# Kernel optimization log

Measured on AMD Instinct MI355X. Metric: run time of the kernel, lower is better.

The kernel has to match this reference:

```python
import jax, jax.numpy as jnp
import numpy as np

N_NODES = 100000
N_EDGES = 1600000
IN_F = 128
OUT_F = 64


def setup_inputs() -> dict:
    key = jax.random.key(0)
    ks = jax.random.split(key, 9)
    x = jax.random.normal(ks[0], (N_NODES, IN_F), dtype=jnp.float32)
    Wv = jax.random.normal(ks[1], (IN_F, OUT_F), dtype=jnp.float32) / np.sqrt(IN_F)
    bv = jax.random.normal(ks[2], (OUT_F,), dtype=jnp.float32) * 0.02
    wq = jax.random.normal(ks[3], (OUT_F,), dtype=jnp.float32) / np.sqrt(OUT_F)
    bq = jax.random.normal(ks[4], (1,), dtype=jnp.float32) * 0.02
    wk = jax.random.normal(ks[5], (OUT_F,), dtype=jnp.float32) / np.sqrt(OUT_F)
    bk = jax.random.normal(ks[6], (1,), dtype=jnp.float32) * 0.02
    src = jax.random.randint(ks[7], (N_EDGES,), 0, N_NODES, dtype=jnp.int64)
    dst = jax.random.randint(ks[8], (N_EDGES,), 0, N_NODES, dtype=jnp.int64)
    return {"x": x, "Wv": Wv, "bv": bv, "wq": wq, "bq": bq,
            "wk": wk, "bk": bk, "src": src, "dst": dst}


def reference(x, Wv, bv, wq, bq, wk, bk, src, dst):
    n = x.shape[0]
    # node transform (linear_v) and scalar scores (linear_q, linear_k)
    xv = x @ Wv + bv                      # [N, OUT_F]
    el = xv @ wq + bq[0]                  # [N] source score
    er = xv @ wk + bk[0]                  # [N] destination score
    # per-edge score: u_add_v + leaky_relu(0.2)
    e = jax.nn.leaky_relu(el[src] + er[dst], negative_slope=0.2)  # [E]
    # edge softmax over incoming edges of each dst (numerically stable)
    emax = jax.ops.segment_max(e, dst, num_segments=n)            # [N]
    ex = jnp.exp(e - emax[dst])                                   # [E]
    denom = jax.ops.segment_sum(ex, dst, num_segments=n)          # [N]
    attn = ex / denom[dst]                                        # [E]
    # u_mul_e + aggregate_sum: weighted scatter of source features into dst
    out = jax.ops.segment_sum(xv[src] * attn[:, None], dst, num_segments=n)
    return out
```

## Files before the change

kernel.cpp:

```cpp
#include <hip/hip_runtime.h>
#include <hip/hip_bf16.h>

#define NN 100000
#define NE 1600000
#define IN_F 128
#define OUT_F 64
#define NBINS 196
#define BIN_SHIFT 9
#define P1_WGS 391
#define NREP2 8
#define SUBCAP 1280

typedef __attribute__((ext_vector_type(8))) short bf16x8;
typedef __attribute__((ext_vector_type(4))) float f32x4;

__device__ __forceinline__ short f2bf(float f) {
  unsigned u = __float_as_uint(f);
  unsigned r = (u + 0x7fffu + ((u >> 16) & 1u)) >> 16;
  return (short)r;
}
__device__ __forceinline__ float bf2f(ushort u) {
  return __uint_as_float(((unsigned)u) << 16);
}

__global__ __launch_bounds__(256) void prep_w(
    const float* __restrict__ Wv, short* __restrict__ wvt) {
  const int i = blockIdx.x * 256 + threadIdx.x;
  if (i >= IN_F * OUT_F) return;
  const int j = i >> 7, k = i & 127;
  wvt[i] = f2bf(Wv[k * OUT_F + j]);
}

__global__ __launch_bounds__(256) void node_transform(
    const float* __restrict__ x, const short* __restrict__ wvt,
    const float* __restrict__ bv, const float* __restrict__ wq,
    const float* __restrict__ bq, const float* __restrict__ wk,
    const float* __restrict__ bk,
    ushort* __restrict__ xvb, float* __restrict__ el, float* __restrict__ er) {
  const int wave = threadIdx.x >> 6, lane = threadIdx.x & 63;
  const int node0 = blockIdx.x * 64 + wave * 16;
  const int j15 = lane & 15, g = lane >> 4;
  const int kb = g * 8;

  int row = node0 + j15;
  if (row >= NN) row = NN - 1;
  const float* xr = x + (size_t)row * IN_F;
  bf16x8 a[4];
#pragma unroll
  for (int kt = 0; kt < 4; ++kt) {
    const float4 f0 = *(const float4*)(xr + kt * 32 + kb);
    const float4 f1 = *(const float4*)(xr + kt * 32 + kb + 4);
    bf16x8 t;
    t[0] = f2bf(f0.x); t[1] = f2bf(f0.y); t[2] = f2bf(f0.z); t[3] = f2bf(f0.w);
    t[4] = f2bf(f1.x); t[5] = f2bf(f1.y); t[6] = f2bf(f1.z); t[7] = f2bf(f1.w);
    a[kt] = t;
  }

  bf16x8 b[16];
#pragma unroll
  for (int nt = 0; nt < 4; ++nt)
#pragma unroll
    for (int kt = 0; kt < 4; ++kt)
      b[nt * 4 + kt] = *(const bf16x8*)(wvt + (size_t)(nt * 16 + j15) * IN_F + kt * 32 + kb);

  f32x4 acc[4];
#pragma unroll
  for (int nt = 0; nt < 4; ++nt) acc[nt] = (f32x4){0.f, 0.f, 0.f, 0.f};
#pragma unroll
  for (int nt = 0; nt < 4; ++nt)
#pragma unroll
    for (int kt = 0; kt < 4; ++kt)
      acc[nt] = __builtin_amdgcn_mfma_f32_16x16x32_bf16(a[kt], b[nt * 4 + kt], acc[nt], 0, 0, 0);

  float bvl[4], wql[4], wkl[4];
#pragma unroll
  for (int nt = 0; nt < 4; ++nt) {
    bvl[nt] = bv[nt * 16 + j15];
    wql[nt] = wq[nt * 16 + j15];
    wkl[nt] = wk[nt * 16 + j15];
  }
  const float bq0 = bq[0], bk0 = bk[0];

#pragma unroll
  for (int r = 0; r < 4; ++r) {
    const int node = node0 + g * 4 + r;
    float pq = 0.f, pk = 0.f;
#pragma unroll
    for (int nt = 0; nt < 4; ++nt) {
      const float v = acc[nt][r] + bvl[nt];
      if (node < NN) xvb[(size_t)node * OUT_F + nt * 16 + j15] = (ushort)f2bf(v);
      pq += v * wql[nt];
      pk += v * wkl[nt];
    }
#pragma unroll
    for (int o = 1; o < 16; o <<= 1) {
      pq += __shfl_xor(pq, o);
      pk += __shfl_xor(pk, o);
    }
    if (j15 == 0 && node < NN) {
      el[node] = pq + bq0;
      er[node] = pk + bk0;
    }
  }
}

__global__ __launch_bounds__(256) void bin_pass1(
    const int* __restrict__ src, const int* __restrict__ dst,
    int* __restrict__ bincur, unsigned* __restrict__ slab) {
  __shared__ int hist[NBINS];
  __shared__ int base_[NBINS];
  const int t = threadIdx.x;
  const int rep = blockIdx.x & (NREP2 - 1);
  for (int i = t; i < NBINS; i += 256) hist[i] = 0;
  __syncthreads();
  const int e0 = blockIdx.x * 4096;
  int sv[16], dv[16];
#pragma unroll
  for (int r = 0; r < 16; ++r) {
    const int i = e0 + r * 256 + t;
    if (i < NE) {
      sv[r] = src[i];
      dv[r] = dst[i];
      atomicAdd(&hist[dv[r] >> BIN_SHIFT], 1);
    } else {
      sv[r] = -1;
      dv[r] = 0;
    }
  }
  __syncthreads();
  for (int b = t; b < NBINS; b += 256) {
    base_[b] = (hist[b] > 0) ? atomicAdd(&bincur[rep * NBINS + b], hist[b]) : 0;
    hist[b] = 0;
  }
  __syncthreads();
#pragma unroll
  for (int r = 0; r < 16; ++r) {
    if (sv[r] >= 0) {
      const int s = sv[r], d = dv[r];
      const int b = d >> BIN_SHIFT;
      const unsigned dl = (unsigned)(d & 511);
      const int pos = base_[b] + atomicAdd(&hist[b], 1);
      slab[(size_t)(b * NREP2 + rep) * SUBCAP + pos] = (dl << 17) | (unsigned)s;
    }
  }
}

__global__ __launch_bounds__(256) void bin_off_k(
    const int* __restrict__ bincur, int* __restrict__ binoff,
    int* __restrict__ off) {
  __shared__ int sp[256];
  const int t = threadIdx.x;
  int v = 0;
  if (t < NBINS) {
#pragma unroll
    for (int r = 0; r < NREP2; ++r) v += bincur[r * NBINS + t];
  }
  sp[t] = v;
  __syncthreads();
  for (int o = 1; o < 256; o <<= 1) {
    const int u = (t >= o) ? sp[t - o] : 0;
    __syncthreads();
    sp[t] += u;
    __syncthreads();
  }
  const int excl = sp[t] - v;
  if (t < NBINS) binoff[t] = excl;
  if (t == 0) { binoff[NBINS] = NE; off[NN] = NE; }
}

__global__ __launch_bounds__(256) void bin_scatter(
    const unsigned* __restrict__ slab, const int* __restrict__ bincur,
    const int* __restrict__ binoff, const float* __restrict__ el,
    const float* __restrict__ er, int* __restrict__ off,
    uint2* __restrict__ csr) {
  __shared__ int cnt2[512];
  __shared__ int sp[256];
  __shared__ float er_l[512];
  const int b = blockIdx.x, t = threadIdx.x;
  const int n0 = b << BIN_SHIFT;
  const int csr0 = binoff[b];

  cnt2[t] = 0; cnt2[t + 256] = 0;
  {
    const int n = n0 + t;
    er_l[t] = (n < NN) ? er[n] : 0.f;
    const int n2 = n0 + 256 + t;
    er_l[256 + t] = (n2 < NN) ? er[n2] : 0.f;
  }
  __syncthreads();

#pragma unroll
  for (int rep = 0; rep < NREP2; ++rep) {
    const int cnt = bincur[rep * NBINS + b];
    const unsigned* sl = slab + (size_t)(b * NREP2 + rep) * SUBCAP;
    for (int i = t; i < cnt; i += 256)
      atomicAdd(&cnt2[sl[i] >> 17], 1);
  }
  __syncthreads();

  const int c0 = cnt2[2 * t], c1 = cnt2[2 * t + 1];
  const int psum = c0 + c1;
  sp[t] = psum;
  __syncthreads();
  for (int o = 1; o < 256; o <<= 1) {
    const int u = (t >= o) ? sp[t - o] : 0;
    __syncthreads();
    sp[t] += u;
    __syncthreads();
  }
  const int excl = sp[t] - psum;
  const int cur0 = csr0 + excl, cur1 = csr0 + excl + c0;
  cnt2[2 * t] = cur0;
  cnt2[2 * t + 1] = cur1;
  if (n0 + 2 * t < NN) off[n0 + 2 * t] = cur0;
  if (n0 + 2 * t + 1 < NN) off[n0 + 2 * t + 1] = cur1;
  __syncthreads();

#pragma unroll
  for (int rep = 0; rep < NREP2; ++rep) {
    const int cnt = bincur[rep * NBINS + b];
    const unsigned* sl = slab + (size_t)(b * NREP2 + rep) * SUBCAP;
    for (int i = t; i < cnt; i += 256) {
      const unsigned w = sl[i];
      const int dl = (int)(w >> 17);
      const int s = (int)(w & 0x1FFFFu);
      float e = el[s] + er_l[dl];
      e = e > 0.f ? e : 0.2f * e;
      const int pos = atomicAdd(&cnt2[dl], 1);
      csr[pos] = (uint2){(unsigned)s, __float_as_uint(e)};
    }
  }
}

__global__ __launch_bounds__(256) void node_aggregate(
    const ushort* __restrict__ xvb, const int* __restrict__ off,
    const uint2* __restrict__ csr, float* __restrict__ out) {
  const int wave = threadIdx.x >> 6, lane = threadIdx.x & 63;
  const int node = blockIdx.x * 4 + wave;
  if (node >= NN) return;
  const int base = off[node];
  const int deg = off[node + 1] - base;

  if (deg <= 64) {
    const bool valid = lane < deg;
    uint2 w = valid ? csr[base + lane] : (uint2){0u, 0u};
    int s = (int)w.x;
    float p = valid ? __expf(__uint_as_float(w.y)) : 0.f;
    float t = p;
#pragma unroll
    for (int o = 32; o; o >>= 1) t += __shfl_xor(t, o);
    p *= (deg > 0) ? (1.0f / t) : 0.f;

    const int fgrp = lane & 7, egrp = lane >> 3;
    float4 aLo = {0.f, 0.f, 0.f, 0.f};
    float4 aHi = {0.f, 0.f, 0.f, 0.f};
    const int nr = (deg + 7) >> 3;
#pragma unroll 4
    for (int r = 0; r < nr; ++r) {
      const int k = (r << 3) + egrp;
      const int sk = __shfl(s, k);
      const float pk = __shfl(p, k);
      if (k < deg) {
        const uint4 v = *(const uint4*)(xvb + (size_t)sk * OUT_F + (fgrp << 3));
        aLo.x += pk * __uint_as_float(v.x << 16);
        aLo.y += pk * __uint_as_float(v.x & 0xffff0000u);
        aLo.z += pk * __uint_as_float(v.y << 16);
        aLo.w += pk * __uint_as_float(v.y & 0xffff0000u);
        aHi.x += pk * __uint_as_float(v.z << 16);
        aHi.y += pk * __uint_as_float(v.z & 0xffff0000u);
        aHi.z += pk * __uint_as_float(v.w << 16);
        aHi.w += pk * __uint_as_float(v.w & 0xffff0000u);
      }
    }
#pragma unroll
    for (int o = 8; o <= 32; o <<= 1) {
      aLo.x += __shfl_xor(aLo.x, o);
      aLo.y += __shfl_xor(aLo.y, o);
      aLo.z += __shfl_xor(aLo.z, o);
      aLo.w += __shfl_xor(aLo.w, o);
      aHi.x += __shfl_xor(aHi.x, o);
      aHi.y += __shfl_xor(aHi.y, o);
      aHi.z += __shfl_xor(aHi.z, o);
      aHi.w += __shfl_xor(aHi.w, o);
    }
    if (egrp == 0) {
      float* op = out + (size_t)node * OUT_F + (fgrp << 3);
      *(float4*)op = aLo;
      *(float4*)(op + 4) = aHi;
    }
  } else {
    float m = -3.0e38f;
    for (int k = lane; k < deg; k += 64) m = fmaxf(m, __uint_as_float(csr[base + k].y));
#pragma unroll
    for (int o = 32; o; o >>= 1) m = fmaxf(m, __shfl_xor(m, o));
    float ssum = 0.f;
    for (int k = lane; k < deg; k += 64) ssum += __expf(__uint_as_float(csr[base + k].y) - m);
#pragma unroll
    for (int o = 32; o; o >>= 1) ssum += __shfl_xor(ssum, o);
    const float inv = 1.0f / ssum;
    float acc = 0.f;
    for (int k = 0; k < deg; ++k) {
      const uint2 w = csr[base + k];
      const float pk = __expf(__uint_as_float(w.y) - m) * inv;
      acc += pk * bf2f(xvb[(size_t)w.x * OUT_F + lane]);
    }
    out[(size_t)node * OUT_F + lane] = acc;
  }
}

extern "C" void kernel_launch(void* const* d_in, const int* in_sizes, int n_in,
                              void* d_out, int out_size, void* d_ws, size_t ws_size,
                              hipStream_t stream) {
  const float* x  = (const float*)d_in[0];
  const float* Wv = (const float*)d_in[1];
  const float* bv = (const float*)d_in[2];
  const float* wq = (const float*)d_in[3];
  const float* bq = (const float*)d_in[4];
  const float* wk = (const float*)d_in[5];
  const float* bk = (const float*)d_in[6];
  const int* src  = (const int*)d_in[7];
  const int* dst  = (const int*)d_in[8];
  float* out = (float*)d_out;

  ushort* xvb = (ushort*)d_ws;
  float* el = (float*)(xvb + (size_t)NN * OUT_F);
  float* er = el + NN;
  int* off = (int*)(er + NN);
  uint2* csr = (uint2*)(off + NN + 2);
  unsigned* slab = (unsigned*)(csr + NE);
  short* wvt = (short*)(slab + (size_t)NBINS * NREP2 * SUBCAP);
  int* bincur = (int*)(wvt + IN_F * OUT_F);
  int* binoff = bincur + NREP2 * NBINS;

  hipMemsetAsync(bincur, 0, NREP2 * NBINS * sizeof(int), stream);

  prep_w<<<(IN_F * OUT_F + 255) / 256, 256, 0, stream>>>(Wv, wvt);
  node_transform<<<(NN + 63) / 64, 256, 0, stream>>>(x, wvt, bv, wq, bq, wk, bk,
                                                     xvb, el, er);
  bin_pass1<<<P1_WGS, 256, 0, stream>>>(src, dst, bincur, slab);
  bin_off_k<<<1, 256, 0, stream>>>(bincur, binoff, off);
  bin_scatter<<<NBINS, 256, 0, stream>>>(slab, bincur, binoff, el, er, off, csr);
  node_aggregate<<<(NN + 3) / 4, 256, 0, stream>>>(xvb, off, csr, out);
}
```

Measured before the change: 132.3 us.

## Fuse node transform with edge binning and fold bin offsets into scatter

```diff
diff --git a/kernel.cpp b/kernel.cpp
--- a/kernel.cpp
+++ b/kernel.cpp
@@ -7,6 +7,7 @@
 #define OUT_F 64
 #define NBINS 196
 #define BIN_SHIFT 9
+#define GEMM_WGS 1563
 #define P1_WGS 391
 #define NREP2 8
 #define SUBCAP 1280
@@ -31,12 +32,55 @@
   wvt[i] = f2bf(Wv[k * OUT_F + j]);
 }
 
-__global__ __launch_bounds__(256) void node_transform(
+__global__ __launch_bounds__(256) void fused_tp(
     const float* __restrict__ x, const short* __restrict__ wvt,
     const float* __restrict__ bv, const float* __restrict__ wq,
     const float* __restrict__ bq, const float* __restrict__ wk,
     const float* __restrict__ bk,
-    ushort* __restrict__ xvb, float* __restrict__ el, float* __restrict__ er) {
+    ushort* __restrict__ xvb, float* __restrict__ el, float* __restrict__ er,
+    const int* __restrict__ src, const int* __restrict__ dst,
+    int* __restrict__ bincur, unsigned* __restrict__ slab) {
+  if (blockIdx.x >= GEMM_WGS) {
+    __shared__ int hist[NBINS];
+    __shared__ int base_[NBINS];
+    const int pb = blockIdx.x - GEMM_WGS;
+    const int t = threadIdx.x;
+    const int rep = pb & (NREP2 - 1);
+    for (int i = t; i < NBINS; i += 256) hist[i] = 0;
+    __syncthreads();
+    const int e0 = pb * 4096;
+    int sv[16], dv[16];
+#pragma unroll
+    for (int r = 0; r < 16; ++r) {
+      const int i = e0 + r * 256 + t;
+      if (i < NE) {
+        sv[r] = src[i];
+        dv[r] = dst[i];
+        atomicAdd(&hist[dv[r] >> BIN_SHIFT], 1);
+      } else {
+        sv[r] = -1;
+        dv[r] = 0;
+      }
+    }
+    __syncthreads();
+    for (int b = t; b < NBINS; b += 256) {
+      base_[b] = (hist[b] > 0) ? atomicAdd(&bincur[rep * NBINS + b], hist[b]) : 0;
+      hist[b] = 0;
+    }
+    __syncthreads();
+#pragma unroll
+    for (int r = 0; r < 16; ++r) {
+      if (sv[r] >= 0) {
+        const int s = sv[r], d = dv[r];
+        const int b = d >> BIN_SHIFT;
+        const unsigned dl = (unsigned)(d & 511);
+        const int pos = base_[b] + atomicAdd(&hist[b], 1);
+        slab[(size_t)(b * NREP2 + rep) * SUBCAP + pos] = (dl << 17) | (unsigned)s;
+      }
+    }
+    return;
+  }
+
   const int wave = threadIdx.x >> 6, lane = threadIdx.x & 63;
   const int node0 = blockIdx.x * 64 + wave * 16;
   const int j15 = lane & 15, g = lane >> 4;
@@ -104,81 +148,31 @@
   }
 }
 
-__global__ __launch_bounds__(256) void bin_pass1(
-    const int* __restrict__ src, const int* __restrict__ dst,
-    int* __restrict__ bincur, unsigned* __restrict__ slab) {
-  __shared__ int hist[NBINS];
-  __shared__ int base_[NBINS];
-  const int t = threadIdx.x;
-  const int rep = blockIdx.x & (NREP2 - 1);
-  for (int i = t; i < NBINS; i += 256) hist[i] = 0;
-  __syncthreads();
-  const int e0 = blockIdx.x * 4096;
-  int sv[16], dv[16];
-#pragma unroll
-  for (int r = 0; r < 16; ++r) {
-    const int i = e0 + r * 256 + t;
-    if (i < NE) {
-      sv[r] = src[i];
-      dv[r] = dst[i];
-      atomicAdd(&hist[dv[r] >> BIN_SHIFT], 1);
-    } else {
-      sv[r] = -1;
-      dv[r] = 0;
-    }
-  }
-  __syncthreads();
-  for (int b = t; b < NBINS; b += 256) {
-    base_[b] = (hist[b] > 0) ? atomicAdd(&bincur[rep * NBINS + b], hist[b]) : 0;
-    hist[b] = 0;
-  }
-  __syncthreads();
-#pragma unroll
-  for (int r = 0; r < 16; ++r) {
-    if (sv[r] >= 0) {
-      const int s = sv[r], d = dv[r];
-      const int b = d >> BIN_SHIFT;
-      const unsigned dl = (unsigned)(d & 511);
-      const int pos = base_[b] + atomicAdd(&hist[b], 1);
-      slab[(size_t)(b * NREP2 + rep) * SUBCAP + pos] = (dl << 17) | (unsigned)s;
-    }
-  }
-}
-
-__global__ __launch_bounds__(256) void bin_off_k(
-    const int* __restrict__ bincur, int* __restrict__ binoff,
-    int* __restrict__ off) {
-  __shared__ int sp[256];
-  const int t = threadIdx.x;
-  int v = 0;
-  if (t < NBINS) {
-#pragma unroll
-    for (int r = 0; r < NREP2; ++r) v += bincur[r * NBINS + t];
-  }
-  sp[t] = v;
-  __syncthreads();
-  for (int o = 1; o < 256; o <<= 1) {
-    const int u = (t >= o) ? sp[t - o] : 0;
-    __syncthreads();
-    sp[t] += u;
-    __syncthreads();
-  }
-  const int excl = sp[t] - v;
-  if (t < NBINS) binoff[t] = excl;
-  if (t == 0) { binoff[NBINS] = NE; off[NN] = NE; }
-}
-
 __global__ __launch_bounds__(256) void bin_scatter(
     const unsigned* __restrict__ slab, const int* __restrict__ bincur,
-    const int* __restrict__ binoff, const float* __restrict__ el,
-    const float* __restrict__ er, int* __restrict__ off,
-    uint2* __restrict__ csr) {
+    const float* __restrict__ el, const float* __restrict__ er,
+    int* __restrict__ off, uint2* __restrict__ csr) {
   __shared__ int cnt2[512];
   __shared__ int sp[256];
   __shared__ float er_l[512];
   const int b = blockIdx.x, t = threadIdx.x;
   const int n0 = b << BIN_SHIFT;
-  const int csr0 = binoff[b];
+
+  int tot = 0;
+  if (t < NBINS) {
+#pragma unroll
+    for (int r = 0; r < NREP2; ++r) tot += bincur[r * NBINS + t];
+  }
+  sp[t] = tot;
+  __syncthreads();
+  for (int o = 1; o < 256; o <<= 1) {
+    const int u = (t >= o) ? sp[t - o] : 0;
+    __syncthreads();
+    sp[t] += u;
+    __syncthreads();
+  }
+  const int csr0 = (b > 0) ? sp[b - 1] : 0;
+  __syncthreads();
 
   cnt2[t] = 0; cnt2[t + 256] = 0;
   {
@@ -214,6 +208,7 @@
   cnt2[2 * t + 1] = cur1;
   if (n0 + 2 * t < NN) off[n0 + 2 * t] = cur0;
   if (n0 + 2 * t + 1 < NN) off[n0 + 2 * t + 1] = cur1;
+  if (b == NBINS - 1 && t == 0) off[NN] = NE;
   __syncthreads();
 
 #pragma unroll
@@ -330,15 +325,12 @@
   unsigned* slab = (unsigned*)(csr + NE);
   short* wvt = (short*)(slab + (size_t)NBINS * NREP2 * SUBCAP);
   int* bincur = (int*)(wvt + IN_F * OUT_F);
-  int* binoff = bincur + NREP2 * NBINS;
 
   hipMemsetAsync(bincur, 0, NREP2 * NBINS * sizeof(int), stream);
 
   prep_w<<<(IN_F * OUT_F + 255) / 256, 256, 0, stream>>>(Wv, wvt);
-  node_transform<<<(NN + 63) / 64, 256, 0, stream>>>(x, wvt, bv, wq, bq, wk, bk,
-                                                     xvb, el, er);
-  bin_pass1<<<P1_WGS, 256, 0, stream>>>(src, dst, bincur, slab);
-  bin_off_k<<<1, 256, 0, stream>>>(bincur, binoff, off);
-  bin_scatter<<<NBINS, 256, 0, stream>>>(slab, bincur, binoff, el, er, off, csr);
+  fused_tp<<<GEMM_WGS + P1_WGS, 256, 0, stream>>>(x, wvt, bv, wq, bq, wk, bk,
+                                                  xvb, el, er, src, dst, bincur, slab);
+  bin_scatter<<<NBINS, 256, 0, stream>>>(slab, bincur, el, er, off, csr);
   node_aggregate<<<(NN + 3) / 4, 256, 0, stream>>>(xvb, off, csr, out);
 }
```

New measurement: 123.6 us. 1.07x faster.
